# Kernel tuning notes

Hardware: AMD Instinct MI355X
Metric: run time of the kernel (lower is better)

The kernel has to match this reference:

```python
import jax, jax.numpy as jnp
import numpy as np

N_NODES = 100000
IN_CH = 128
HID = 128   # 2 * out_channels
OUT = 64
N_EDGES = 1600000


def gcn_conv(x, W, b, src, dst, n_nodes):
    """PyG GCNConv: add self-loops, symmetric normalization D^-1/2 (A+I) D^-1/2 X W + b."""
    h = x @ W  # [N, F_out]
    ones = jnp.ones(dst.shape[0], dtype=h.dtype)
    # degree of target nodes, +1 for self loop
    deg = jax.ops.segment_sum(ones, dst, num_segments=n_nodes) + 1.0
    dinv = jnp.where(deg > 0, jax.lax.rsqrt(deg), 0.0)  # [N]
    norm = dinv[src] * dinv[dst]  # [E]
    agg = jax.ops.segment_sum(h[src] * norm[:, None], dst, num_segments=n_nodes)
    # self-loop contribution: norm_ii = dinv_i^2 (avoids materializing extra edges)
    agg = agg + h * (dinv * dinv)[:, None]
    return agg + b


def setup_inputs() -> dict:
    key = jax.random.key(0)
    ks = jax.random.split(key, 8)
    x = jax.random.normal(ks[0], (N_NODES, IN_CH), dtype=jnp.float32)
    edge_index = jax.random.randint(ks[1], (2, N_EDGES), 0, N_NODES, dtype=jnp.int64)
    # Glorot-style params
    W1 = jax.random.normal(ks[2], (IN_CH, HID), dtype=jnp.float32) / np.sqrt(IN_CH)
    b1 = jnp.zeros((HID,), dtype=jnp.float32)
    W_mu = jax.random.normal(ks[3], (HID, OUT), dtype=jnp.float32) / np.sqrt(HID)
    b_mu = jnp.zeros((OUT,), dtype=jnp.float32)
    W_ls = jax.random.normal(ks[4], (HID, OUT), dtype=jnp.float32) / np.sqrt(HID)
    b_ls = jnp.zeros((OUT,), dtype=jnp.float32)
    return {"x": x, "edge_index": edge_index, "W1": W1, "b1": b1,
            "W_mu": W_mu, "b_mu": b_mu, "W_ls": W_ls, "b_ls": b_ls}


def reference(x, edge_index, W1, b1, W_mu, b_mu, W_ls, b_ls):
    src, dst = edge_index[0], edge_index[1]
    n = x.shape[0]
    h = jax.nn.relu(gcn_conv(x, W1, b1, src, dst, n))
    mu = gcn_conv(h, W_mu, b_mu, src, dst, n)
    logstd = gcn_conv(h, W_ls, b_ls, src, dst, n)
    return (mu, logstd)
```

## Files before the change

kernel.cpp:

```cpp
#include <hip/hip_runtime.h>
#include <hip/hip_bf16.h>
#include <stdint.h>

#define N_NODES 100000
#define IN_CH   128
#define HID     128
#define OUT_CH  64
#define N_EDGES 1600000

#define NB    196
#define NBLK  250
#define EPB   6400

typedef __attribute__((ext_vector_type(8))) short  bf16x8;
typedef __attribute__((ext_vector_type(4))) float  f32x4;


__device__ __forceinline__ unsigned short f2bf(float f) {
    unsigned int u = __float_as_uint(f);
    u = (u + 0x7fffu + ((u >> 16) & 1u)) >> 16;
    return (unsigned short)u;
}
__device__ __forceinline__ float bfl(unsigned int u) { return __uint_as_float(u << 16); }
__device__ __forceinline__ float bfh(unsigned int u) { return __uint_as_float(u & 0xffff0000u); }


__global__ __launch_bounds__(256) void k_phaseA(const int* __restrict__ dst,
                                                int* __restrict__ Cm) {
    __shared__ int hist[NB];
    int blk = blockIdx.x, t = threadIdx.x;
    if (t < NB) hist[t] = 0;
    __syncthreads();
    int base = blk * EPB;
#pragma unroll 5
    for (int k = 0; k < EPB / 256; k++) {
        int d = dst[base + k * 256 + t];
        atomicAdd(&hist[d >> 9], 1);
    }
    __syncthreads();
    if (t < NB) Cm[blk * NB + t] = hist[t];
}

__global__ __launch_bounds__(256) void k_scanBkt(int* __restrict__ Cm,
                                                 int* __restrict__ bktSum) {
    __shared__ int sdata[256];
    int b = blockIdx.x, t = threadIdx.x;
    int v = (t < NBLK) ? Cm[t * NB + b] : 0;
    sdata[t] = v;
    __syncthreads();
    int val = v;
    for (int off = 1; off < 256; off <<= 1) {
        int tmp = (t >= off) ? sdata[t - off] : 0;
        __syncthreads();
        val += tmp;
        sdata[t] = val;
        __syncthreads();
    }
    if (t < NBLK) Cm[t * NB + b] = val - v;
    if (t == 255) bktSum[b] = val;
}

__global__ __launch_bounds__(256) void k_scanBase(const int* __restrict__ bktSum,
                                                  int* __restrict__ bktBase) {
    __shared__ int sdata[256];
    int t = threadIdx.x;
    int v = (t < NB) ? bktSum[t] : 0;
    sdata[t] = v;
    __syncthreads();
    int val = v;
    for (int off = 1; off < 256; off <<= 1) {
        int tmp = (t >= off) ? sdata[t - off] : 0;
        __syncthreads();
        val += tmp;
        sdata[t] = val;
        __syncthreads();
    }
    if (t < NB) bktBase[t] = val - v;
    if (t == 0) bktBase[NB] = N_EDGES;
}

__global__ __launch_bounds__(256) void k_phaseB(const int* __restrict__ src,
                                                const int* __restrict__ dst,
                                                const int* __restrict__ Cm,
                                                const int* __restrict__ bktBase,
                                                unsigned int* __restrict__ bucketed) {
    __shared__ int offs[NB];
    int blk = blockIdx.x, t = threadIdx.x;
    if (t < NB) offs[t] = Cm[blk * NB + t] + bktBase[t];
    __syncthreads();
    int base = blk * EPB;
#pragma unroll 5
    for (int k = 0; k < EPB / 256; k++) {
        int e = base + k * 256 + t;
        int d = dst[e];
        int sv = src[e];
        int pos = atomicAdd(&offs[d >> 9], 1);
        bucketed[pos] = ((unsigned int)sv << 9) | (unsigned int)(d & 511);
    }
}

__global__ __launch_bounds__(512) void k_phaseC(const unsigned int* __restrict__ bucketed,
                                                const int* __restrict__ bktBase,
                                                int* __restrict__ rowptr,
                                                float* __restrict__ dinvg,
                                                int* __restrict__ csr_src) {
    __shared__ int cnt[512];
    __shared__ int cur[512];
    __shared__ int sdata[512];
    int b = blockIdx.x, t = threadIdx.x;
    int base = bktBase[b], endR = bktBase[b + 1];
    int nodeBase = b << 9;
    int nNodes = N_NODES - nodeBase;
    if (nNodes > 512) nNodes = 512;

    cnt[t] = 0;
    __syncthreads();
    for (int e = base + t; e < endR; e += 512)
        atomicAdd(&cnt[bucketed[e] & 511], 1);
    __syncthreads();

    int s = cnt[t];
    sdata[t] = s;
    __syncthreads();
    int val = s;
    for (int off = 1; off < 512; off <<= 1) {
        int tmp = (t >= off) ? sdata[t - off] : 0;
        __syncthreads();
        val += tmp;
        sdata[t] = val;
        __syncthreads();
    }
    cur[t] = val - s;
    if (t < nNodes) {
        rowptr[nodeBase + t] = base + val - s;
        dinvg[nodeBase + t] = rsqrtf((float)s + 1.0f);
    }
    if (b == NB - 1 && t == 0) rowptr[N_NODES] = N_EDGES;
    __syncthreads();

    for (int e = base + t; e < endR; e += 512) {
        unsigned int u = bucketed[e];
        int pos = base + atomicAdd(&cur[u & 511], 1);
        csr_src[pos] = (int)(u >> 9);
    }
}


__global__ __launch_bounds__(256) void k_prepW(const float* __restrict__ W1,
                                               const float* __restrict__ Wmu,
                                               const float* __restrict__ Wls,
                                               unsigned short* __restrict__ Wt1,
                                               unsigned short* __restrict__ WtC) {
    int idx = blockIdx.x * 256 + threadIdx.x;
    int n = idx >> 7, k = idx & 127;
    Wt1[idx] = f2bf(W1[k * 128 + n]);
    WtC[idx] = f2bf((n < 64) ? Wmu[k * 64 + n] : Wls[k * 64 + (n - 64)]);
}


#define LDA 136

__global__ __launch_bounds__(256) void k_gemm1(const float* __restrict__ X,
                                               const unsigned short* __restrict__ Wt,
                                               const float* __restrict__ dinv,
                                               unsigned short* __restrict__ Y) {
    __shared__ unsigned short sA[128 * LDA];
    int t = threadIdx.x;
    int R0 = blockIdx.x * 128;
    int row = t >> 1, colb = (t & 1) * 64;
    bool valid = (R0 + row) < N_NODES;
    const float* Xr = X + (size_t)(R0 + row) * 128 + colb;
    unsigned short* dp = sA + row * LDA + colb;
#pragma unroll
    for (int j = 0; j < 16; j++) {
        float4 v = valid ? *(const float4*)(Xr + j * 4) : make_float4(0.f, 0.f, 0.f, 0.f);
        ushort4 o;
        o.x = f2bf(v.x); o.y = f2bf(v.y); o.z = f2bf(v.z); o.w = f2bf(v.w);
        *(ushort4*)(dp + j * 4) = o;
    }
    __syncthreads();

    int wv = t >> 6, l = t & 63;
    int quad = l >> 4, lm = l & 15;

    bf16x8 a[2][4];
#pragma unroll
    for (int mt = 0; mt < 2; mt++)
#pragma unroll
        for (int ks = 0; ks < 4; ks++)
            a[mt][ks] = *(const bf16x8*)(sA + (wv * 32 + mt * 16 + lm) * LDA +
                                         ks * 32 + quad * 8);

    f32x4 acc[2][8] = {};
#pragma unroll
    for (int nt = 0; nt < 8; nt++) {
        bf16x8 b[4];
        const unsigned short* Wp = Wt + (nt * 16 + lm) * 128 + quad * 8;
#pragma unroll
        for (int ks = 0; ks < 4; ks++)
            b[ks] = *(const bf16x8*)(Wp + ks * 32);
#pragma unroll
        for (int mt = 0; mt < 2; mt++) {
            f32x4 c = acc[mt][nt];
#pragma unroll
            for (int ks = 0; ks < 4; ks++)
                c = __builtin_amdgcn_mfma_f32_16x16x32_bf16(a[mt][ks], b[ks], c, 0, 0, 0);
            acc[mt][nt] = c;
        }
    }

    int rbase = R0 + wv * 32 + quad * 4;
    float dv[2][4];
#pragma unroll
    for (int mt = 0; mt < 2; mt++)
#pragma unroll
        for (int reg = 0; reg < 4; reg++) {
            int r = rbase + mt * 16 + reg;
            dv[mt][reg] = (r < N_NODES) ? dinv[r] : 0.f;
        }
#pragma unroll
    for (int mt = 0; mt < 2; mt++)
#pragma unroll
        for (int nt = 0; nt < 8; nt++)
#pragma unroll
            for (int reg = 0; reg < 4; reg++) {
                int r = rbase + mt * 16 + reg;
                if (r < N_NODES)
                    Y[(size_t)r * 128 + nt * 16 + lm] = f2bf(acc[mt][nt][reg] * dv[mt][reg]);
            }
}


__global__ __launch_bounds__(256) void k_agg1(const unsigned short* __restrict__ h0,
                                              const int* __restrict__ rowptr,
                                              const int* __restrict__ csr_src,
                                              const float* __restrict__ dinv,
                                              const float* __restrict__ b1,
                                              unsigned short* __restrict__ hb) {
    int t = threadIdx.x;
    int wv = t >> 6, lane = t & 63;
    int nodeBase = blockIdx.x * 16;
    int c2 = lane * 2;

#pragma unroll 1
    for (int j4 = 0; j4 < 4; j4++) {
        int i = __builtin_amdgcn_readfirstlane(nodeBase + wv * 4 + j4);
        float di = dinv[i];
        unsigned int sv = *(const unsigned int*)(h0 + (size_t)i * 128 + c2);
        float ax = bfl(sv), ay = bfh(sv);
        int beg = rowptr[i], end = rowptr[i + 1];
        for (int p = beg; p < end; p += 32) {
            int s[32]; unsigned int r[32];
#pragma unroll
            for (int j = 0; j < 32; j++) {
                int q = p + j;
                s[j] = __builtin_nontemporal_load(csr_src + (q < end ? q : end - 1));
            }
#pragma unroll
            for (int j = 0; j < 32; j++)
                r[j] = *(const unsigned int*)(h0 + (size_t)s[j] * 128 + c2);
#pragma unroll
            for (int j = 0; j < 32; j++) {
                unsigned int v = (p + j < end) ? r[j] : 0u;
                ax += bfl(v);
                ay += bfh(v);
            }
        }
        ax = ax * di + b1[c2];
        ay = ay * di + b1[c2 + 1];
        ax = ax > 0.f ? ax : 0.f;
        ay = ay > 0.f ? ay : 0.f;
        ax *= di;
        ay *= di;
        unsigned int pk = ((unsigned int)f2bf(ay) << 16) | (unsigned int)f2bf(ax);
        *(unsigned int*)(hb + (size_t)i * 128 + c2) = pk;
    }
}


#define LDG 136

__global__ __launch_bounds__(256) void k_agg2g(const unsigned short* __restrict__ hb,
                                               const int* __restrict__ rowptr,
                                               const int* __restrict__ csr_src,
                                               const float* __restrict__ dinv,
                                               const unsigned short* __restrict__ WtC,
                                               const float* __restrict__ bmu,
                                               const float* __restrict__ bls,
                                               float* __restrict__ out) {
    __shared__ unsigned short g[16 * LDG];
    int t = threadIdx.x;
    int wv = t >> 6, lane = t & 63;
    int nodeBase = blockIdx.x * 16;
    int c2 = lane * 2;

#pragma unroll 1
    for (int j4 = 0; j4 < 4; j4++) {
        int i = __builtin_amdgcn_readfirstlane(nodeBase + wv * 4 + j4);
        float di = dinv[i];
        unsigned int sv = *(const unsigned int*)(hb + (size_t)i * 128 + c2);
        float ax = bfl(sv), ay = bfh(sv);
        int beg = rowptr[i], end = rowptr[i + 1];
        for (int p = beg; p < end; p += 32) {
            int s[32]; unsigned int r[32];
#pragma unroll
            for (int j = 0; j < 32; j++) {
                int q = p + j;
                s[j] = __builtin_nontemporal_load(csr_src + (q < end ? q : end - 1));
            }
#pragma unroll
            for (int j = 0; j < 32; j++)
                r[j] = *(const unsigned int*)(hb + (size_t)s[j] * 128 + c2);
#pragma unroll
            for (int j = 0; j < 32; j++) {
                unsigned int v = (p + j < end) ? r[j] : 0u;
                ax += bfl(v);
                ay += bfh(v);
            }
        }
        ax *= di;
        ay *= di;
        unsigned int pk = ((unsigned int)f2bf(ay) << 16) | (unsigned int)f2bf(ax);
        *(unsigned int*)(g + (wv * 4 + j4) * LDG + c2) = pk;
    }
    __syncthreads();

    int quad = lane >> 4, lm = lane & 15;
    bf16x8 a[4];
#pragma unroll
    for (int ks = 0; ks < 4; ks++)
        a[ks] = *(const bf16x8*)(g + lm * LDG + ks * 32 + quad * 8);

#pragma unroll
    for (int nt2 = 0; nt2 < 2; nt2++) {
        int nt = wv * 2 + nt2;
        f32x4 acc = {};
        const unsigned short* Wp = WtC + (nt * 16 + lm) * 128 + quad * 8;
#pragma unroll
        for (int ks = 0; ks < 4; ks++) {
            bf16x8 b = *(const bf16x8*)(Wp + ks * 32);
            acc = __builtin_amdgcn_mfma_f32_16x16x32_bf16(a[ks], b, acc, 0, 0, 0);
        }
        int col = nt * 16 + lm;
#pragma unroll
        for (int reg = 0; reg < 4; reg++) {
            int row = nodeBase + quad * 4 + reg;
            float v = acc[reg];
            if (col < 64)
                out[(size_t)row * 64 + col] = v + bmu[col];
            else
                out[(size_t)N_NODES * 64 + (size_t)row * 64 + (col - 64)] = v + bls[col - 64];
        }
    }
}


extern "C" void kernel_launch(void* const* d_in, const int* in_sizes, int n_in,
                              void* d_out, int out_size, void* d_ws, size_t ws_size,
                              hipStream_t stream) {
    const float* x    = (const float*)d_in[0];
    const int*   ei   = (const int*)d_in[1];
    const float* W1   = (const float*)d_in[2];
    const float* b1   = (const float*)d_in[3];
    const float* Wmu  = (const float*)d_in[4];
    const float* bmu  = (const float*)d_in[5];
    const float* Wls  = (const float*)d_in[6];
    const float* bls  = (const float*)d_in[7];
    const int* src = ei;
    const int* dst = ei + N_EDGES;

    char* p = (char*)d_ws;
    unsigned short* bufA = (unsigned short*)p; p += (size_t)N_NODES * 128 * 2;
    unsigned short* bufH = (unsigned short*)p; p += (size_t)N_NODES * 128 * 2;
    unsigned short* Wt1  = (unsigned short*)p; p += 128 * 128 * 2;
    unsigned short* WtC  = (unsigned short*)p; p += 128 * 128 * 2;
    int*   Cm      = (int*)p;   p += (size_t)NBLK * NB * 4;
    int*   bktSum  = (int*)p;   p += 256 * 4;
    int*   bktBase = (int*)p;   p += 256 * 4;
    int*   rowptr  = (int*)p;   p += 400016;
    float* dinv    = (float*)p; p += 400000;
    unsigned int* bucketed = (unsigned int*)p; p += (size_t)N_EDGES * 4;
    int*   csr_src = (int*)p;   p += (size_t)N_EDGES * 4;

    k_phaseA<<<NBLK, 256, 0, stream>>>(dst, Cm);
    k_scanBkt<<<NB, 256, 0, stream>>>(Cm, bktSum);
    k_scanBase<<<1, 256, 0, stream>>>(bktSum, bktBase);
    k_phaseB<<<NBLK, 256, 0, stream>>>(src, dst, Cm, bktBase, bucketed);
    k_phaseC<<<NB, 512, 0, stream>>>(bucketed, bktBase, rowptr, dinv, csr_src);

    k_prepW<<<64, 256, 0, stream>>>(W1, Wmu, Wls, Wt1, WtC);

    int gblk = (N_NODES + 127) / 128;

    k_gemm1<<<gblk, 256, 0, stream>>>(x, Wt1, dinv, bufA);
    k_agg1<<<N_NODES / 16, 256, 0, stream>>>(bufA, rowptr, csr_src, dinv, b1, bufH);

    k_agg2g<<<N_NODES / 16, 256, 0, stream>>>(bufH, rowptr, csr_src, dinv,
                                              WtC, bmu, bls, (float*)d_out);
}
```

Measured before the change: 352.2 us.

## Fuse bucket histogram and scatter using global atomics and fixed-capacity buckets

Replaces the histogram, per-bucket scan, base scan and scatter kernels with a single kernel that reserves per-bucket offsets via global atomics and writes edges into fixed-capacity bucket slabs. The phase C kernel now computes bucket base offsets itself with a block scan over the bucket counts. This removes several kernel launches and the Cm matrix traffic. In exchange it relies on no bucket exceeding the fixed capacity, and edge order within a row becomes nondeterministic.

```diff
diff --git a/kernel.cpp b/kernel.cpp
--- a/kernel.cpp
+++ b/kernel.cpp
@@ -11,6 +11,7 @@
 #define NB    196
 #define NBLK  250
 #define EPB   6400
+#define CAP   10240
 
 typedef __attribute__((ext_vector_type(8))) short  bf16x8;
 typedef __attribute__((ext_vector_type(4))) float  f32x4;
@@ -25,8 +26,10 @@
 __device__ __forceinline__ float bfh(unsigned int u) { return __uint_as_float(u & 0xffff0000u); }
 
 
-__global__ __launch_bounds__(256) void k_phaseA(const int* __restrict__ dst,
-                                                int* __restrict__ Cm) {
+__global__ __launch_bounds__(256) void k_scatter1(const int* __restrict__ src,
+                                                  const int* __restrict__ dst,
+                                                  int* __restrict__ bucketCnt,
+                                                  unsigned int* __restrict__ bucketed) {
     __shared__ int hist[NB];
     int blk = blockIdx.x, t = threadIdx.x;
     if (t < NB) hist[t] = 0;
@@ -38,85 +41,56 @@
         atomicAdd(&hist[d >> 9], 1);
     }
     __syncthreads();
-    if (t < NB) Cm[blk * NB + t] = hist[t];
-}
-
-__global__ __launch_bounds__(256) void k_scanBkt(int* __restrict__ Cm,
-                                                 int* __restrict__ bktSum) {
-    __shared__ int sdata[256];
-    int b = blockIdx.x, t = threadIdx.x;
-    int v = (t < NBLK) ? Cm[t * NB + b] : 0;
-    sdata[t] = v;
-    __syncthreads();
-    int val = v;
-    for (int off = 1; off < 256; off <<= 1) {
-        int tmp = (t >= off) ? sdata[t - off] : 0;
-        __syncthreads();
-        val += tmp;
-        sdata[t] = val;
-        __syncthreads();
-    }
-    if (t < NBLK) Cm[t * NB + b] = val - v;
-    if (t == 255) bktSum[b] = val;
-}
-
-__global__ __launch_bounds__(256) void k_scanBase(const int* __restrict__ bktSum,
-                                                  int* __restrict__ bktBase) {
-    __shared__ int sdata[256];
-    int t = threadIdx.x;
-    int v = (t < NB) ? bktSum[t] : 0;
-    sdata[t] = v;
-    __syncthreads();
-    int val = v;
-    for (int off = 1; off < 256; off <<= 1) {
-        int tmp = (t >= off) ? sdata[t - off] : 0;
-        __syncthreads();
-        val += tmp;
-        sdata[t] = val;
-        __syncthreads();
-    }
-    if (t < NB) bktBase[t] = val - v;
-    if (t == 0) bktBase[NB] = N_EDGES;
-}
-
-__global__ __launch_bounds__(256) void k_phaseB(const int* __restrict__ src,
-                                                const int* __restrict__ dst,
-                                                const int* __restrict__ Cm,
-                                                const int* __restrict__ bktBase,
-                                                unsigned int* __restrict__ bucketed) {
-    __shared__ int offs[NB];
-    int blk = blockIdx.x, t = threadIdx.x;
-    if (t < NB) offs[t] = Cm[blk * NB + t] + bktBase[t];
-    __syncthreads();
-    int base = blk * EPB;
+    if (t < NB) hist[t] = atomicAdd(&bucketCnt[t], hist[t]);
+    __syncthreads();
 #pragma unroll 5
     for (int k = 0; k < EPB / 256; k++) {
         int e = base + k * 256 + t;
         int d = dst[e];
         int sv = src[e];
-        int pos = atomicAdd(&offs[d >> 9], 1);
-        bucketed[pos] = ((unsigned int)sv << 9) | (unsigned int)(d & 511);
-    }
-}
+        int pos = atomicAdd(&hist[d >> 9], 1);
+        bucketed[(size_t)(d >> 9) * CAP + pos] =
+            ((unsigned int)sv << 9) | (unsigned int)(d & 511);
+    }
+}
+
 
 __global__ __launch_bounds__(512) void k_phaseC(const unsigned int* __restrict__ bucketed,
-                                                const int* __restrict__ bktBase,
+                                                const int* __restrict__ bucketCnt,
                                                 int* __restrict__ rowptr,
                                                 float* __restrict__ dinvg,
                                                 int* __restrict__ csr_src) {
     __shared__ int cnt[512];
     __shared__ int cur[512];
     __shared__ int sdata[512];
+    __shared__ int s_base, s_cnt;
     int b = blockIdx.x, t = threadIdx.x;
-    int base = bktBase[b], endR = bktBase[b + 1];
+
+    int bv = (t < NB) ? bucketCnt[t] : 0;
+    sdata[t] = bv;
+    __syncthreads();
+    int bval = bv;
+    for (int off = 1; off < 512; off <<= 1) {
+        int tmp = (t >= off) ? sdata[t - off] : 0;
+        __syncthreads();
+        bval += tmp;
+        sdata[t] = bval;
+        __syncthreads();
+    }
+    if (t == b) { s_base = bval - bv; s_cnt = bv; }
+    __syncthreads();
+    int base = s_base;
+    int nEdge = s_cnt;
+
+    const unsigned int* bk = bucketed + (size_t)b * CAP;
     int nodeBase = b << 9;
     int nNodes = N_NODES - nodeBase;
     if (nNodes > 512) nNodes = 512;
 
     cnt[t] = 0;
     __syncthreads();
-    for (int e = base + t; e < endR; e += 512)
-        atomicAdd(&cnt[bucketed[e] & 511], 1);
+    for (int e = t; e < nEdge; e += 512)
+        atomicAdd(&cnt[bk[e] & 511], 1);
     __syncthreads();
 
     int s = cnt[t];
@@ -138,8 +112,8 @@
     if (b == NB - 1 && t == 0) rowptr[N_NODES] = N_EDGES;
     __syncthreads();
 
-    for (int e = base + t; e < endR; e += 512) {
-        unsigned int u = bucketed[e];
+    for (int e = t; e < nEdge; e += 512) {
+        unsigned int u = bk[e];
         int pos = base + atomicAdd(&cur[u & 511], 1);
         csr_src[pos] = (int)(u >> 9);
     }
@@ -374,19 +348,15 @@
     unsigned short* bufH = (unsigned short*)p; p += (size_t)N_NODES * 128 * 2;
     unsigned short* Wt1  = (unsigned short*)p; p += 128 * 128 * 2;
     unsigned short* WtC  = (unsigned short*)p; p += 128 * 128 * 2;
-    int*   Cm      = (int*)p;   p += (size_t)NBLK * NB * 4;
-    int*   bktSum  = (int*)p;   p += 256 * 4;
-    int*   bktBase = (int*)p;   p += 256 * 4;
+    int*   bucketCnt = (int*)p; p += 256 * 4;
     int*   rowptr  = (int*)p;   p += 400016;
     float* dinv    = (float*)p; p += 400000;
-    unsigned int* bucketed = (unsigned int*)p; p += (size_t)N_EDGES * 4;
+    unsigned int* bucketed = (unsigned int*)p; p += (size_t)NB * CAP * 4;
     int*   csr_src = (int*)p;   p += (size_t)N_EDGES * 4;
 
-    k_phaseA<<<NBLK, 256, 0, stream>>>(dst, Cm);
-    k_scanBkt<<<NB, 256, 0, stream>>>(Cm, bktSum);
-    k_scanBase<<<1, 256, 0, stream>>>(bktSum, bktBase);
-    k_phaseB<<<NBLK, 256, 0, stream>>>(src, dst, Cm, bktBase, bucketed);
-    k_phaseC<<<NB, 512, 0, stream>>>(bucketed, bktBase, rowptr, dinv, csr_src);
+    hipMemsetAsync(bucketCnt, 0, NB * sizeof(int), stream);
+    k_scatter1<<<NBLK, 256, 0, stream>>>(src, dst, bucketCnt, bucketed);
+    k_phaseC<<<NB, 512, 0, stream>>>(bucketed, bucketCnt, rowptr, dinv, csr_src);
 
     k_prepW<<<64, 256, 0, stream>>>(W1, Wmu, Wls, Wt1, WtC);
 
```

After: 347.9 us. No clear change (-1.2%).
